# Kernel optimization log

Hardware: AMD Instinct MI355X
Metric: run time of the kernel (lower is better)

The kernel has to match this reference:

```python
import jax, jax.numpy as jnp
import numpy as np

N1, N2, F = 512, 512, 128
H = 512  # hidden width


def _xavier(key, shape):
    fan_in, fan_out = shape
    std = (2.0 / (fan_in + fan_out)) ** 0.5
    return jax.random.normal(key, shape, dtype=jnp.float32) * std


def setup_inputs() -> dict:
    key = jax.random.key(0)
    ks = jax.random.split(key, 8)
    V1 = jax.random.normal(ks[0], (1, N1, F), dtype=jnp.float32)
    V2 = jax.random.normal(ks[1], (1, N2, F), dtype=jnp.float32)
    W1 = _xavier(ks[2], (2 * F, H))
    b1 = 0.0001 + 5e-05 * jax.random.normal(ks[3], (H,), dtype=jnp.float32)
    W2 = _xavier(ks[4], (H, H))
    b2 = 0.0001 + 5e-05 * jax.random.normal(ks[5], (H,), dtype=jnp.float32)
    W3 = _xavier(ks[6], (H, 2))
    b3 = 0.0001 + 5e-05 * jax.random.normal(ks[7], (2,), dtype=jnp.float32)
    return {"V1": V1, "V2": V2, "W1": W1, "b1": b1, "W2": W2, "b2": b2, "W3": W3, "b3": b3}


def reference(V1, V2, W1, b1, W2, b2, W3, b3):
    n1, n2, f = V1.shape[1], V2.shape[1], V1.shape[2]
    # Fused broadcast-concat replacing the N1*N2 Python double loop
    # (i outer, j inner; V1[i] first, V2[j] second -> row-major reshape matches stack order)
    pairs = jnp.concatenate([
        jnp.broadcast_to(V1[0][:, None, :], (n1, n2, f)),
        jnp.broadcast_to(V2[0][None, :, :], (n1, n2, f)),
    ], axis=-1).reshape(1, n1 * n2, 2 * f)
    h = jax.nn.relu(pairs @ W1 + b1)
    h = jax.nn.relu(h @ W2 + b2)
    out = jax.nn.relu(h @ W3 + b3)  # final LinearEmbedding also has ReLU by default
    return out
```

## Files before the change

kernel.cpp:

```cpp
#include <hip/hip_runtime.h>


typedef short bf16x8 __attribute__((ext_vector_type(8)));
typedef float f32x16 __attribute__((ext_vector_type(16)));

#define NROW 512
#define FDIM 128
#define HDIM 512

__device__ __forceinline__ unsigned int pk2(float x, float y) {
  unsigned int r;
  asm("v_cvt_pk_bf16_f32 %0, %1, %2" : "=v"(r) : "v"(x), "v"(y));
  return r;
}
__device__ __forceinline__ unsigned short f2bf(float x) {
  unsigned int u = __builtin_bit_cast(unsigned int, x);
  u += 0x7fffu + ((u >> 16) & 1u);
  return (unsigned short)(u >> 16);
}
__device__ __forceinline__ float bflo(unsigned int u) {
  return __builtin_bit_cast(float, u << 16);
}
__device__ __forceinline__ float bfhi(unsigned int u) {
  return __builtin_bit_cast(float, u & 0xffff0000u);
}

__global__ __launch_bounds__(256) void prep_fused(
    const float* __restrict__ V1, const float* __restrict__ V2,
    const float* __restrict__ W1, const float* __restrict__ b1,
    const float* __restrict__ W2, float* __restrict__ Ap,
    unsigned short* __restrict__ Bpb, unsigned short* __restrict__ W2T) {
  const int b = blockIdx.x;
  const int t = threadIdx.x;
  if (b >= 256) {
    const int o = (b - 256) * 256 + t;
    const int kc = o >> 9;
    const int n = o & 511;
    unsigned int u[4];
#pragma unroll
    for (int e2 = 0; e2 < 4; ++e2)
      u[e2] = pk2(W2[(kc * 8 + 2 * e2) * HDIM + n], W2[(kc * 8 + 2 * e2 + 1) * HDIM + n]);
    *(uint4*)(W2T + (size_t)o * 8) = make_uint4(u[0], u[1], u[2], u[3]);
    return;
  }
  __shared__ float sv[4 * FDIM];
  const bool isB = b >= 128;
  const int r0 = (b & 127) * 4;
  const float* V = isB ? V2 : V1;
  const float* W = W1 + (isB ? FDIM * HDIM : 0);
  for (int idx = t; idx < 4 * FDIM; idx += 256) sv[idx] = V[r0 * FDIM + idx];
  __syncthreads();
  float s[4][2] = {};
  for (int k = 0; k < FDIM; ++k) {
    const float w0 = W[k * HDIM + t];
    const float w1 = W[k * HDIM + t + 256];
#pragma unroll
    for (int r = 0; r < 4; ++r) {
      const float v = sv[r * FDIM + k];
      s[r][0] += v * w0;
      s[r][1] += v * w1;
    }
  }
  if (isB) {
#pragma unroll
    for (int r = 0; r < 4; ++r) {
      Bpb[(r0 + r) * HDIM + t] = f2bf(s[r][0]);
      Bpb[(r0 + r) * HDIM + t + 256] = f2bf(s[r][1]);
    }
  } else {
    const float bb0 = b1[t];
    const float bb1 = b1[t + 256];
#pragma unroll
    for (int r = 0; r < 4; ++r) {
      Ap[(r0 + r) * HDIM + t] = s[r][0] + bb0;
      Ap[(r0 + r) * HDIM + t + 256] = s[r][1] + bb1;
    }
  }
}

__global__ __launch_bounds__(512, 2) void mlp_main(
    const float* __restrict__ Ap, const unsigned short* __restrict__ Bpb,
    const unsigned short* __restrict__ W2T, const float* __restrict__ b2,
    const float* __restrict__ W3, const float* __restrict__ b3,
    float* __restrict__ out) {
  extern __shared__ char smem[];
  char* sA = smem;

  const int tid = threadIdx.x;
  const int wave = tid >> 6;
  const int lane = tid & 63;
  const int cl = lane & 31;
  const int hi = lane >> 5;
  const int r15 = lane & 15;

  const int m0 = blockIdx.x * 128;
  const int i = m0 >> 9;
  const int j0 = m0 & 511;

  const char* bbase = (const char*)W2T + (((wave << 6) + cl) << 4) + (hi << 13);

  bf16x8 af[2][4], bfr[5][2];
#pragma unroll
  for (int q = 0; q < 4; ++q) {
    const char* bp = bbase + ((size_t)q << 14);
    bfr[q][0] = *(const bf16x8*)(bp);
    bfr[q][1] = *(const bf16x8*)(bp + (1 << 9));
  }
  float w30[2], w31[2], bb[2];
#pragma unroll
  for (int nt = 0; nt < 2; ++nt) {
    const int n = (wave << 6) + (nt << 5) + cl;
    w30[nt] = W3[2 * n];
    w31[nt] = W3[2 * n + 1];
    bb[nt] = b2[n];
  }
  const float bb3_0 = b3[0], bb3_1 = b3[1];

  {
    const int c = tid & 63;
    const int rsub = tid >> 6;
    const float4 a0 = *(const float4*)(Ap + i * HDIM + c * 8);
    const float4 a1 = *(const float4*)(Ap + i * HDIM + c * 8 + 4);
#pragma unroll
    for (int it = 0; it < 16; ++it) {
      const int row = it * 8 + rsub;
      const uint4 ub = *(const uint4*)(Bpb + (size_t)(j0 + row) * HDIM + c * 8);
      const uint4 v = make_uint4(
          pk2(fmaxf(a0.x + bflo(ub.x), 0.f), fmaxf(a0.y + bfhi(ub.x), 0.f)),
          pk2(fmaxf(a0.z + bflo(ub.y), 0.f), fmaxf(a0.w + bfhi(ub.y), 0.f)),
          pk2(fmaxf(a1.x + bflo(ub.z), 0.f), fmaxf(a1.y + bfhi(ub.z), 0.f)),
          pk2(fmaxf(a1.z + bflo(ub.w), 0.f), fmaxf(a1.w + bfhi(ub.w), 0.f)));
      *(uint4*)(sA + row * 1024 + ((c ^ (row & 15)) << 4)) = v;
    }
  }
  __syncthreads();

  f32x16 acc[4][2];
#pragma unroll
  for (int mt = 0; mt < 4; ++mt)
#pragma unroll
    for (int nt = 0; nt < 2; ++nt)
#pragma unroll
      for (int q = 0; q < 16; ++q) acc[mt][nt][q] = 0.f;

  const char* abase0 = sA + cl * 1024;
  {
    const int off = (hi ^ r15) << 4;
#pragma unroll
    for (int mt = 0; mt < 4; ++mt) af[0][mt] = *(const bf16x8*)(abase0 + mt * 32768 + off);
  }
#pragma unroll
  for (int s = 0; s < 32; ++s) {
    const int cur = s & 1;
    if (s < 31) {
      const int off = ((((s + 1) << 1) | hi) ^ r15) << 4;
#pragma unroll
      for (int mt = 0; mt < 4; ++mt)
        af[cur ^ 1][mt] = *(const bf16x8*)(abase0 + mt * 32768 + off);
    }
    if (s < 28) {
      const char* bp = bbase + ((size_t)(s + 4) << 14);
      bfr[(s + 4) % 5][0] = *(const bf16x8*)(bp);
      bfr[(s + 4) % 5][1] = *(const bf16x8*)(bp + (1 << 9));
    }
    __builtin_amdgcn_s_setprio(1);
#pragma unroll
    for (int nt = 0; nt < 2; ++nt)
#pragma unroll
      for (int mt = 0; mt < 4; ++mt)
        acc[mt][nt] = __builtin_amdgcn_mfma_f32_32x32x16_bf16(af[cur][mt], bfr[s % 5][nt],
                                                              acc[mt][nt], 0, 0, 0);
    __builtin_amdgcn_s_setprio(0);
  }

  __syncthreads();

#pragma unroll
  for (int rnd = 0; rnd < 2; ++rnd) {
#pragma unroll
    for (int ml = 0; ml < 2; ++ml) {
      const int mt = rnd * 2 + ml;
      char* ebuf = smem + ml * 65536;
#pragma unroll
      for (int rp = 0; rp < 8; ++rp) {
        const int ra = 2 * rp;
        const float h0a = fmaxf(acc[mt][0][ra] + bb[0], 0.f);
        const float h1a = fmaxf(acc[mt][1][ra] + bb[1], 0.f);
        const float h0b = fmaxf(acc[mt][0][ra + 1] + bb[0], 0.f);
        const float h1b = fmaxf(acc[mt][1][ra + 1] + bb[1], 0.f);
        const float4 v =
            make_float4(h0a * w30[0] + h1a * w30[1], h0a * w31[0] + h1a * w31[1],
                        h0b * w30[0] + h1b * w30[1], h0b * w31[0] + h1b * w31[1]);
        const int rpi = ((ra & 3) + 8 * (ra >> 2) + 4 * hi) >> 1;
        *(float4*)(ebuf + rpi * 4096 + (((wave << 5) + cl) << 4)) = v;
      }
    }
    __syncthreads();
    {
      const int ml = tid >> 8;
      const int t2 = tid & 255;
      const int rpi = t2 >> 4;
      const int sub = t2 & 15;
      const char* ebuf = smem + ml * 65536;
      float4 s4 = make_float4(0.f, 0.f, 0.f, 0.f);
#pragma unroll
      for (int k = 0; k < 16; ++k) {
        const float4 v = *(const float4*)(ebuf + rpi * 4096 + ((sub + (k << 4)) << 4));
        s4.x += v.x; s4.y += v.y; s4.z += v.z; s4.w += v.w;
      }
#pragma unroll
      for (int d = 1; d < 16; d <<= 1) {
        s4.x += __shfl_xor(s4.x, d, 64);
        s4.y += __shfl_xor(s4.y, d, 64);
        s4.z += __shfl_xor(s4.z, d, 64);
        s4.w += __shfl_xor(s4.w, d, 64);
      }
      if (sub == 0) {
        const int rg = m0 + ((rnd * 2 + ml) << 5) + (rpi << 1);
        *(float4*)(out + rg * 2) =
            make_float4(fmaxf(s4.x + bb3_0, 0.f), fmaxf(s4.y + bb3_1, 0.f),
                        fmaxf(s4.z + bb3_0, 0.f), fmaxf(s4.w + bb3_1, 0.f));
      }
    }
    __syncthreads();
  }
}

extern "C" void kernel_launch(void* const* d_in, const int* in_sizes, int n_in,
                              void* d_out, int out_size, void* d_ws, size_t ws_size,
                              hipStream_t stream) {
  const float* V1 = (const float*)d_in[0];
  const float* V2 = (const float*)d_in[1];
  const float* W1 = (const float*)d_in[2];
  const float* b1 = (const float*)d_in[3];
  const float* W2 = (const float*)d_in[4];
  const float* b2 = (const float*)d_in[5];
  const float* W3 = (const float*)d_in[6];
  const float* b3 = (const float*)d_in[7];

  float* Ap = (float*)d_ws;
  unsigned short* Bpb = (unsigned short*)(Ap + NROW * HDIM);
  unsigned short* W2T = Bpb + NROW * HDIM;

  const int smem_bytes = 131072;
  (void)hipFuncSetAttribute((const void*)mlp_main,
                            hipFuncAttributeMaxDynamicSharedMemorySize, smem_bytes);

  prep_fused<<<384, 256, 0, stream>>>(V1, V2, W1, b1, W2, Ap, Bpb, W2T);
  mlp_main<<<2048, 512, smem_bytes, stream>>>(Ap, Bpb, W2T, b2, W3, b3, (float*)d_out);
}
```

Before: 143.6 us.

## Split layer-1 A-tile build into two K halves, overlapping second half with MFMA

The shared-memory A tile (relu of Ap+Bp in bf16) is now built in two K halves: the first 256 columns up front, and the second half loaded from global and packed into a separate LDS region while the MFMAs consume the first half. The swizzle changes to a 512-byte row with XOR over 32 chunks. The W2T register prefetch depth drops from 5 to 3 slots to save VGPRs. The aim is to hide the global load and pack latency of the prologue behind tensor-core work, at the cost of an extra barrier and a shallower B prefetch.

```diff
diff --git a/kernel.cpp b/kernel.cpp
--- a/kernel.cpp
+++ b/kernel.cpp
@@ -23,6 +23,12 @@
 }
 __device__ __forceinline__ float bfhi(unsigned int u) {
   return __builtin_bit_cast(float, u & 0xffff0000u);
+}
+__device__ __forceinline__ uint4 packrow(const float4& a0, const float4& a1, const uint4& ub) {
+  return make_uint4(pk2(fmaxf(a0.x + bflo(ub.x), 0.f), fmaxf(a0.y + bfhi(ub.x), 0.f)),
+                    pk2(fmaxf(a0.z + bflo(ub.y), 0.f), fmaxf(a0.w + bfhi(ub.y), 0.f)),
+                    pk2(fmaxf(a1.x + bflo(ub.z), 0.f), fmaxf(a1.y + bfhi(ub.z), 0.f)),
+                    pk2(fmaxf(a1.z + bflo(ub.w), 0.f), fmaxf(a1.w + bfhi(ub.w), 0.f)));
 }
 
 __global__ __launch_bounds__(256) void prep_fused(
@@ -84,14 +90,14 @@
     const float* __restrict__ W3, const float* __restrict__ b3,
     float* __restrict__ out) {
   extern __shared__ char smem[];
-  char* sA = smem;
 
   const int tid = threadIdx.x;
   const int wave = tid >> 6;
   const int lane = tid & 63;
   const int cl = lane & 31;
   const int hi = lane >> 5;
-  const int r15 = lane & 15;
+  const int fc = tid & 31;
+  const int frs = tid >> 5;
 
   const int m0 = blockIdx.x * 128;
   const int i = m0 >> 9;
@@ -99,9 +105,9 @@
 
   const char* bbase = (const char*)W2T + (((wave << 6) + cl) << 4) + (hi << 13);
 
-  bf16x8 af[2][4], bfr[5][2];
-#pragma unroll
-  for (int q = 0; q < 4; ++q) {
+  bf16x8 af[2][4], bfr[3][2];
+#pragma unroll
+  for (int q = 0; q < 2; ++q) {
     const char* bp = bbase + ((size_t)q << 14);
     bfr[q][0] = *(const bf16x8*)(bp);
     bfr[q][1] = *(const bf16x8*)(bp + (1 << 9));
@@ -117,22 +123,17 @@
   const float bb3_0 = b3[0], bb3_1 = b3[1];
 
   {
-    const int c = tid & 63;
-    const int rsub = tid >> 6;
-    const float4 a0 = *(const float4*)(Ap + i * HDIM + c * 8);
-    const float4 a1 = *(const float4*)(Ap + i * HDIM + c * 8 + 4);
-#pragma unroll
-    for (int it = 0; it < 16; ++it) {
-      const int row = it * 8 + rsub;
-      const uint4 ub = *(const uint4*)(Bpb + (size_t)(j0 + row) * HDIM + c * 8);
-      const uint4 v = make_uint4(
-          pk2(fmaxf(a0.x + bflo(ub.x), 0.f), fmaxf(a0.y + bfhi(ub.x), 0.f)),
-          pk2(fmaxf(a0.z + bflo(ub.y), 0.f), fmaxf(a0.w + bfhi(ub.y), 0.f)),
-          pk2(fmaxf(a1.x + bflo(ub.z), 0.f), fmaxf(a1.y + bfhi(ub.z), 0.f)),
-          pk2(fmaxf(a1.z + bflo(ub.w), 0.f), fmaxf(a1.w + bfhi(ub.w), 0.f)));
-      *(uint4*)(sA + row * 1024 + ((c ^ (row & 15)) << 4)) = v;
-    }
-  }
+    const float4 a0 = *(const float4*)(Ap + i * HDIM + fc * 8);
+    const float4 a1 = *(const float4*)(Ap + i * HDIM + fc * 8 + 4);
+#pragma unroll
+    for (int it = 0; it < 8; ++it) {
+      const int row = it * 16 + frs;
+      const uint4 ub = *(const uint4*)(Bpb + (size_t)(j0 + row) * HDIM + fc * 8);
+      *(uint4*)(smem + row * 512 + ((fc ^ (row & 31)) << 4)) = packrow(a0, a1, ub);
+    }
+  }
+  const float4 a0n = *(const float4*)(Ap + i * HDIM + 256 + fc * 8);
+  const float4 a1n = *(const float4*)(Ap + i * HDIM + 256 + fc * 8 + 4);
   __syncthreads();
 
   f32x16 acc[4][2];
@@ -143,36 +144,81 @@
 #pragma unroll
       for (int q = 0; q < 16; ++q) acc[mt][nt][q] = 0.f;
 
-  const char* abase0 = sA + cl * 1024;
   {
-    const int off = (hi ^ r15) << 4;
-#pragma unroll
-    for (int mt = 0; mt < 4; ++mt) af[0][mt] = *(const bf16x8*)(abase0 + mt * 32768 + off);
-  }
-#pragma unroll
-  for (int s = 0; s < 32; ++s) {
-    const int cur = s & 1;
-    if (s < 31) {
-      const int off = ((((s + 1) << 1) | hi) ^ r15) << 4;
-#pragma unroll
-      for (int mt = 0; mt < 4; ++mt)
-        af[cur ^ 1][mt] = *(const bf16x8*)(abase0 + mt * 32768 + off);
-    }
-    if (s < 28) {
-      const char* bp = bbase + ((size_t)(s + 4) << 14);
-      bfr[(s + 4) % 5][0] = *(const bf16x8*)(bp);
-      bfr[(s + 4) % 5][1] = *(const bf16x8*)(bp + (1 << 9));
-    }
-    __builtin_amdgcn_s_setprio(1);
-#pragma unroll
-    for (int nt = 0; nt < 2; ++nt)
-#pragma unroll
-      for (int mt = 0; mt < 4; ++mt)
-        acc[mt][nt] = __builtin_amdgcn_mfma_f32_32x32x16_bf16(af[cur][mt], bfr[s % 5][nt],
-                                                              acc[mt][nt], 0, 0, 0);
-    __builtin_amdgcn_s_setprio(0);
-  }
-
+    const char* abase = smem + cl * 512;
+    char* sA1 = smem + 65536;
+    {
+      const int off = (hi ^ cl) << 4;
+#pragma unroll
+      for (int mt = 0; mt < 4; ++mt) af[0][mt] = *(const bf16x8*)(abase + mt * 16384 + off);
+    }
+    uint4 ub;
+    int frow = 0;
+#pragma unroll
+    for (int s = 0; s < 16; ++s) {
+      const int cur = s & 1;
+      if ((s & 1) == 0) {
+        __builtin_amdgcn_sched_barrier(0);
+        frow = (s >> 1) * 16 + frs;
+        ub = *(const uint4*)(Bpb + (size_t)(j0 + frow) * HDIM + 256 + fc * 8);
+      } else {
+        *(uint4*)(sA1 + frow * 512 + ((fc ^ (frow & 31)) << 4)) = packrow(a0n, a1n, ub);
+      }
+      if (s < 15) {
+        const int off = (((((s + 1) << 1) | hi)) ^ cl) << 4;
+#pragma unroll
+        for (int mt = 0; mt < 4; ++mt)
+          af[cur ^ 1][mt] = *(const bf16x8*)(abase + mt * 16384 + off);
+      }
+      {
+        const char* bp = bbase + ((size_t)(s + 2) << 14);
+        bfr[(s + 2) % 3][0] = *(const bf16x8*)(bp);
+        bfr[(s + 2) % 3][1] = *(const bf16x8*)(bp + (1 << 9));
+      }
+      __builtin_amdgcn_s_setprio(1);
+#pragma unroll
+      for (int nt = 0; nt < 2; ++nt)
+#pragma unroll
+        for (int mt = 0; mt < 4; ++mt)
+          acc[mt][nt] = __builtin_amdgcn_mfma_f32_32x32x16_bf16(af[cur][mt], bfr[s % 3][nt],
+                                                                acc[mt][nt], 0, 0, 0);
+      __builtin_amdgcn_s_setprio(0);
+    }
+  }
+  __syncthreads();
+
+  {
+    const char* abase = smem + 65536 + cl * 512;
+    {
+      const int off = (hi ^ cl) << 4;
+#pragma unroll
+      for (int mt = 0; mt < 4; ++mt) af[0][mt] = *(const bf16x8*)(abase + mt * 16384 + off);
+    }
+#pragma unroll
+    for (int sl = 0; sl < 16; ++sl) {
+      const int s = 16 + sl;
+      const int cur = sl & 1;
+      if (sl < 15) {
+        const int off = (((((sl + 1) << 1) | hi)) ^ cl) << 4;
+#pragma unroll
+        for (int mt = 0; mt < 4; ++mt)
+          af[cur ^ 1][mt] = *(const bf16x8*)(abase + mt * 16384 + off);
+      }
+      if (s < 30) {
+        const char* bp = bbase + ((size_t)(s + 2) << 14);
+        bfr[(s + 2) % 3][0] = *(const bf16x8*)(bp);
+        bfr[(s + 2) % 3][1] = *(const bf16x8*)(bp + (1 << 9));
+      }
+      __builtin_amdgcn_s_setprio(1);
+#pragma unroll
+      for (int nt = 0; nt < 2; ++nt)
+#pragma unroll
+        for (int mt = 0; mt < 4; ++mt)
+          acc[mt][nt] = __builtin_amdgcn_mfma_f32_32x32x16_bf16(af[cur][mt], bfr[s % 3][nt],
+                                                                acc[mt][nt], 0, 0, 0);
+      __builtin_amdgcn_s_setprio(0);
+    }
+  }
   __syncthreads();
 
 #pragma unroll
```

Result: no change. 145.0 us (+1.0%).
